# Kernel optimization log

Hardware: AMD Instinct MI355X
Metric: run time of the kernel (lower is better)

Reference implementation:

```python
import jax, jax.numpy as jnp
import numpy as np

NUM_EMBEDDINGS = 512
EMBEDDING_DIM = 64
COMMITMENT_COST = 0.25


def setup_inputs() -> dict:
    key = jax.random.key(0)
    k1, k2 = jax.random.split(key)
    inputs = jax.random.normal(k1, (16, EMBEDDING_DIM, 4096), dtype=jnp.float32)
    # torch init: uniform(-1/num_embeddings, 1/num_embeddings)
    codebook = jax.random.uniform(
        k2, (NUM_EMBEDDINGS, EMBEDDING_DIM), dtype=jnp.float32,
        minval=-1.0 / NUM_EMBEDDINGS, maxval=1.0 / NUM_EMBEDDINGS)
    return {"inputs": inputs, "codebook": codebook}


def reference(inputs, codebook):
    # inputs: [B, D, T] -> permute to [B, T, D]
    x = jnp.transpose(inputs, (0, 2, 1))
    B, T, D = x.shape
    K = codebook.shape[0]
    flat = x.reshape(-1, D)  # [N, D]

    distances = (jnp.sum(flat * flat, axis=1, keepdims=True)
                 + jnp.sum(codebook * codebook, axis=1)
                 - 2.0 * flat @ codebook.T)  # [N, K]
    idx = jnp.argmin(distances, axis=1)  # [N]
    encodings = jax.nn.one_hot(idx, K, dtype=jnp.float32)  # [N, K]

    # direct gather == encodings @ codebook
    quantized = codebook[idx].reshape(B, T, D)

    e_latent_loss = jnp.mean((jax.lax.stop_gradient(quantized) - x) ** 2)
    q_latent_loss = jnp.mean((quantized - jax.lax.stop_gradient(x)) ** 2)
    loss = q_latent_loss + COMMITMENT_COST * e_latent_loss

    # straight-through estimator
    quantized_st = x + jax.lax.stop_gradient(quantized - x)

    avg_probs = jnp.mean(encodings, axis=0)
    perplexity = jnp.exp(-jnp.sum(avg_probs * jnp.log(avg_probs + 1e-10)))

    return (loss, jnp.transpose(quantized_st, (0, 2, 1)), perplexity, encodings)
```

## Files before the change

kernel.cpp:

```cpp
#include <hip/hip_runtime.h>

#define B_ 16
#define D_ 64
#define T_ 4096
#define K_ 512
#define N_ (B_*T_)
#define Q_ (B_*D_*T_)
#define ENC_OFF ((size_t)(2 + Q_))

#define WS_LOSS    0
#define WS_HIST    16
#define WS_NE      2064
#define WS_CBH     4608
#define WS_CBL     70144

typedef __bf16 bf16x8 __attribute__((ext_vector_type(8)));
typedef float  f32x4  __attribute__((ext_vector_type(4)));

__global__ __launch_bounds__(256) void k0_init(const float* __restrict__ cb,
                                               float* __restrict__ ne,
                                               int* __restrict__ hist,
                                               double* __restrict__ loss,
                                               bf16x8* __restrict__ cbh,
                                               bf16x8* __restrict__ cbl) {
    int bidx = blockIdx.x, tid = threadIdx.x;

    if (tid < 64) {
        int code = bidx * 64 + tid;
        float s = 0.f;
#pragma unroll
        for (int d = 0; d < 64; ++d) { float c = cb[code*64 + d]; s = fmaf(c, c, s); }
        ne[code] = s;
    }
    if (bidx == 0) {
        hist[tid] = 0; hist[tid + 256] = 0;
        if (tid == 0) *loss = 0.0;
    }

#pragma unroll
    for (int p = 0; p < 2; ++p) {
        int e = p * 256 + tid;
        int ct = bidx * 4 + (e >> 7);
        int ks = (e >> 6) & 1;
        int lane = e & 63;
        int code  = ct * 16 + (lane & 15);
        int dbase = ks * 32 + ((lane >> 4) << 3);
        bf16x8 h, l;
#pragma unroll
        for (int j = 0; j < 8; ++j) {
            float v = cb[code * 64 + dbase + j];
            __bf16 hv = (__bf16)v;
            __bf16 lv = (__bf16)(v - (float)hv);
            h[j] = hv; l[j] = lv;
        }
        cbh[(ct * 2 + ks) * 64 + lane] = h;
        cbl[(ct * 2 + ks) * 64 + lane] = l;
    }
}

__global__ __launch_bounds__(256) void k_main(const float* __restrict__ in,
                                              const float* __restrict__ cb,
                                              const bf16x8* __restrict__ cbh,
                                              const bf16x8* __restrict__ cbl,
                                              const float* __restrict__ ne,
                                              float* __restrict__ out,
                                              float2* __restrict__ enc2,
                                              int* __restrict__ hist,
                                              double* __restrict__ loss) {
    __shared__ float X[64][65];
    __shared__ float ne_s[512];
    __shared__ int   sidx[64];
    int tid = threadIdx.x;
    int n0 = blockIdx.x * 64;
    int b  = n0 >> 12, t0 = n0 & (T_ - 1);

    {
        int tl = tid & 63, dg = tid >> 6;
#pragma unroll
        for (int i = 0; i < 16; ++i) {
            int d = dg * 16 + i;
            X[d][tl] = in[((size_t)b * 64 + d) * T_ + t0 + tl];
        }
    }
    ne_s[tid] = ne[tid];
    ne_s[tid + 256] = ne[tid + 256];
    __syncthreads();

    int w = tid >> 6, lane = tid & 63;
    int col = lane & 15, q = lane >> 4;

    bf16x8 Ah[2], Al[2];
#pragma unroll
    for (int ks = 0; ks < 2; ++ks) {
        bf16x8 h, l;
#pragma unroll
        for (int j = 0; j < 8; ++j) {
            float v = X[ks * 32 + q * 8 + j][w * 16 + col];
            __bf16 hv = (__bf16)v;
            __bf16 lv = (__bf16)(v - (float)hv);
            h[j] = hv; l[j] = lv;
        }
        Ah[ks] = h; Al[ks] = l;
    }

    float m1[4]; int i1[4];
#pragma unroll
    for (int e = 0; e < 4; ++e) { m1[e] = 3.4e38f; i1[e] = 0; }

    for (int ct = 0; ct < 32; ++ct) {
        bf16x8 Bh0 = cbh[(ct * 2 + 0) * 64 + lane];
        bf16x8 Bh1 = cbh[(ct * 2 + 1) * 64 + lane];
        bf16x8 Bl0 = cbl[(ct * 2 + 0) * 64 + lane];
        bf16x8 Bl1 = cbl[(ct * 2 + 1) * 64 + lane];
        float nev = ne_s[ct * 16 + col];
        int code = ct * 16 + col;
        f32x4 acc = {0.f, 0.f, 0.f, 0.f};
        acc = __builtin_amdgcn_mfma_f32_16x16x32_bf16(Ah[0], Bh0, acc, 0, 0, 0);
        acc = __builtin_amdgcn_mfma_f32_16x16x32_bf16(Ah[1], Bh1, acc, 0, 0, 0);
        acc = __builtin_amdgcn_mfma_f32_16x16x32_bf16(Ah[0], Bl0, acc, 0, 0, 0);
        acc = __builtin_amdgcn_mfma_f32_16x16x32_bf16(Al[0], Bh0, acc, 0, 0, 0);
        acc = __builtin_amdgcn_mfma_f32_16x16x32_bf16(Ah[1], Bl1, acc, 0, 0, 0);
        acc = __builtin_amdgcn_mfma_f32_16x16x32_bf16(Al[1], Bh1, acc, 0, 0, 0);
#pragma unroll
        for (int e = 0; e < 4; ++e) {
            float sc = fmaf(-2.f, acc[e], nev);
            bool lt = sc < m1[e];
            i1[e] = lt ? code : i1[e];
            m1[e] = lt ? sc : m1[e];
        }
    }

#pragma unroll
    for (int e = 0; e < 4; ++e) {
        float a1 = m1[e]; int ai = i1[e];
#pragma unroll
        for (int off = 1; off < 16; off <<= 1) {
            float o1 = __shfl_xor(a1, off);
            int   oi = __shfl_xor(ai, off);
            bool tk = (o1 < a1) || (o1 == a1 && oi < ai);
            a1 = tk ? o1 : a1; ai = tk ? oi : ai;
        }
        if (col == 0) sidx[w * 16 + q * 4 + e] = ai;
    }
    __syncthreads();

#pragma unroll 4
    for (int i = 0; i < 64; ++i) {
        int id = sidx[i];
        float2 v;
        v.x = ((id >> 1) == tid && (id & 1) == 0) ? 1.f : 0.f;
        v.y = ((id >> 1) == tid && (id & 1) == 1) ? 1.f : 0.f;
        enc2[(size_t)(n0 + i) * 256 + tid] = v;
    }

    int tl = tid & 63, dg = tid >> 6;
    int idq = sidx[tl];
    const float4* cq4 = (const float4*)(cb + (size_t)idq * 64 + dg * 16);
    float* qp = out + 1 + (size_t)b * D_ * T_ + (size_t)(dg * 16) * T_ + t0 + tl;

    float lsum = 0.f;
#pragma unroll
    for (int j4 = 0; j4 < 4; ++j4) {
        float4 qv = cq4[j4];
        float qe[4] = {qv.x, qv.y, qv.z, qv.w};
#pragma unroll
        for (int e = 0; e < 4; ++e) {
            int dl = j4 * 4 + e;
            float xv = X[dg * 16 + dl][tl];
            float diff = qe[e] - xv;
            lsum = fmaf(diff, diff, lsum);
            qp[(size_t)dl * T_] = xv + diff;
        }
    }
    if (tid < 64) atomicAdd(&hist[idq], 1);

#pragma unroll
    for (int off = 32; off > 0; off >>= 1) lsum += __shfl_down(lsum, off);
    __shared__ float wsum[4];
    if ((tid & 63) == 0) wsum[tid >> 6] = lsum;
    __syncthreads();
    if (tid == 0) {
        double s = (double)wsum[0] + (double)wsum[1] + (double)wsum[2] + (double)wsum[3];
        atomicAdd(loss, s);
    }
}

__global__ __launch_bounds__(512) void k6_final(const int* __restrict__ hist,
                                                const double* __restrict__ loss,
                                                float* __restrict__ out) {
    __shared__ double sh[512];
    int k = threadIdx.x;
    double p = (double)hist[k] / (double)N_;
    sh[k] = p * log(p + 1e-10);
    __syncthreads();
    for (int s = 256; s > 0; s >>= 1) {
        if (k < s) sh[k] += sh[k + s];
        __syncthreads();
    }
    if (k == 0) {
        out[1 + Q_] = (float)exp(-sh[0]);
        out[0] = (float)(1.25 * (*loss) / (double)Q_);
    }
}

extern "C" void kernel_launch(void* const* d_in, const int* in_sizes, int n_in,
                              void* d_out, int out_size, void* d_ws, size_t ws_size,
                              hipStream_t stream) {
    const float* in = (const float*)d_in[0];
    const float* cb = (const float*)d_in[1];
    float* out = (float*)d_out;
    char* ws = (char*)d_ws;

    double* loss  = (double*)(ws + WS_LOSS);
    int* hist     = (int*)(ws + WS_HIST);
    float* ne     = (float*)(ws + WS_NE);
    bf16x8* cbh   = (bf16x8*)(ws + WS_CBH);
    bf16x8* cbl   = (bf16x8*)(ws + WS_CBL);

    float2* enc2 = (float2*)(out + ENC_OFF);

    k0_init<<<8, 256, 0, stream>>>(cb, ne, hist, loss, cbh, cbl);
    k_main<<<N_ / 64, 256, 0, stream>>>(in, cb, cbh, cbl, ne, out, enc2, hist, loss);
    k6_final<<<1, 512, 0, stream>>>(hist, loss, out);
}
```

Baseline: 197.3 us.

## Replace global atomics with per-block partials and a final-kernel histogram

```diff
diff --git a/kernel.cpp b/kernel.cpp
--- a/kernel.cpp
+++ b/kernel.cpp
@@ -8,54 +8,44 @@
 #define Q_ (B_*D_*T_)
 #define ENC_OFF ((size_t)(2 + Q_))
 
-#define WS_LOSS    0
-#define WS_HIST    16
-#define WS_NE      2064
-#define WS_CBH     4608
-#define WS_CBL     70144
+#define WS_NE    0
+#define WS_LPART 2048
+#define WS_GIDX  6144
+#define WS_CBH   268288
+#define WS_CBL   333824
 
 typedef __bf16 bf16x8 __attribute__((ext_vector_type(8)));
 typedef float  f32x4  __attribute__((ext_vector_type(4)));
 
 __global__ __launch_bounds__(256) void k0_init(const float* __restrict__ cb,
                                                float* __restrict__ ne,
-                                               int* __restrict__ hist,
-                                               double* __restrict__ loss,
                                                bf16x8* __restrict__ cbh,
                                                bf16x8* __restrict__ cbl) {
     int bidx = blockIdx.x, tid = threadIdx.x;
 
-    if (tid < 64) {
-        int code = bidx * 64 + tid;
+    {
+        int code = bidx * 32 + (tid >> 3), sl = tid & 7;
         float s = 0.f;
 #pragma unroll
-        for (int d = 0; d < 64; ++d) { float c = cb[code*64 + d]; s = fmaf(c, c, s); }
-        ne[code] = s;
-    }
-    if (bidx == 0) {
-        hist[tid] = 0; hist[tid + 256] = 0;
-        if (tid == 0) *loss = 0.0;
-    }
-
-#pragma unroll
-    for (int p = 0; p < 2; ++p) {
-        int e = p * 256 + tid;
-        int ct = bidx * 4 + (e >> 7);
-        int ks = (e >> 6) & 1;
-        int lane = e & 63;
-        int code  = ct * 16 + (lane & 15);
-        int dbase = ks * 32 + ((lane >> 4) << 3);
-        bf16x8 h, l;
-#pragma unroll
-        for (int j = 0; j < 8; ++j) {
-            float v = cb[code * 64 + dbase + j];
-            __bf16 hv = (__bf16)v;
-            __bf16 lv = (__bf16)(v - (float)hv);
-            h[j] = hv; l[j] = lv;
-        }
-        cbh[(ct * 2 + ks) * 64 + lane] = h;
-        cbl[(ct * 2 + ks) * 64 + lane] = l;
-    }
+        for (int j = 0; j < 8; ++j) { float c = cb[code * 64 + sl * 8 + j]; s = fmaf(c, c, s); }
+        s += __shfl_xor(s, 1); s += __shfl_xor(s, 2); s += __shfl_xor(s, 4);
+        if (sl == 0) ne[code] = s;
+    }
+
+    int e = bidx * 256 + tid;
+    int ct = e >> 7, ks = (e >> 6) & 1, lane = e & 63;
+    int code  = ct * 16 + (lane & 15);
+    int dbase = ks * 32 + ((lane >> 4) << 3);
+    bf16x8 h, l;
+#pragma unroll
+    for (int j = 0; j < 8; ++j) {
+        float v = cb[code * 64 + dbase + j];
+        __bf16 hv = (__bf16)v;
+        __bf16 lv = (__bf16)(v - (float)hv);
+        h[j] = hv; l[j] = lv;
+    }
+    cbh[(ct * 2 + ks) * 64 + lane] = h;
+    cbl[(ct * 2 + ks) * 64 + lane] = l;
 }
 
 __global__ __launch_bounds__(256) void k_main(const float* __restrict__ in,
@@ -65,8 +55,8 @@
                                               const float* __restrict__ ne,
                                               float* __restrict__ out,
                                               float2* __restrict__ enc2,
-                                              int* __restrict__ hist,
-                                              double* __restrict__ loss) {
+                                              int* __restrict__ gidx,
+                                              float* __restrict__ lpart) {
     __shared__ float X[64][65];
     __shared__ float ne_s[512];
     __shared__ int   sidx[64];
@@ -172,34 +162,42 @@
             qp[(size_t)dl * T_] = xv + diff;
         }
     }
-    if (tid < 64) atomicAdd(&hist[idq], 1);
+    if (tid < 64) gidx[n0 + tid] = idq;
 
 #pragma unroll
     for (int off = 32; off > 0; off >>= 1) lsum += __shfl_down(lsum, off);
     __shared__ float wsum[4];
     if ((tid & 63) == 0) wsum[tid >> 6] = lsum;
     __syncthreads();
-    if (tid == 0) {
-        double s = (double)wsum[0] + (double)wsum[1] + (double)wsum[2] + (double)wsum[3];
-        atomicAdd(loss, s);
-    }
-}
-
-__global__ __launch_bounds__(512) void k6_final(const int* __restrict__ hist,
-                                                const double* __restrict__ loss,
+    if (tid == 0)
+        lpart[blockIdx.x] = wsum[0] + wsum[1] + wsum[2] + wsum[3];
+}
+
+__global__ __launch_bounds__(512) void k6_final(const int* __restrict__ gidx,
+                                                const float* __restrict__ lpart,
                                                 float* __restrict__ out) {
+    __shared__ int    h[512];
     __shared__ double sh[512];
+    __shared__ double sl2[512];
     int k = threadIdx.x;
-    double p = (double)hist[k] / (double)N_;
-    sh[k] = p * log(p + 1e-10);
+    h[k] = 0;
+    __syncthreads();
+#pragma unroll 4
+    for (int i = 0; i < 128; ++i)
+        atomicAdd(&h[gidx[(size_t)i * 512 + k]], 1);
+    double ls = (double)lpart[k] + (double)lpart[k + 512];
+    __syncthreads();
+    double p = (double)h[k] / (double)N_;
+    sh[k]  = p * log(p + 1e-10);
+    sl2[k] = ls;
     __syncthreads();
     for (int s = 256; s > 0; s >>= 1) {
-        if (k < s) sh[k] += sh[k + s];
+        if (k < s) { sh[k] += sh[k + s]; sl2[k] += sl2[k + s]; }
         __syncthreads();
     }
     if (k == 0) {
         out[1 + Q_] = (float)exp(-sh[0]);
-        out[0] = (float)(1.25 * (*loss) / (double)Q_);
+        out[0] = (float)(1.25 * sl2[0] / (double)Q_);
     }
 }
 
@@ -211,15 +209,15 @@
     float* out = (float*)d_out;
     char* ws = (char*)d_ws;
 
-    double* loss  = (double*)(ws + WS_LOSS);
-    int* hist     = (int*)(ws + WS_HIST);
     float* ne     = (float*)(ws + WS_NE);
+    float* lpart  = (float*)(ws + WS_LPART);
+    int*   gidx   = (int*)(ws + WS_GIDX);
     bf16x8* cbh   = (bf16x8*)(ws + WS_CBH);
     bf16x8* cbl   = (bf16x8*)(ws + WS_CBL);
 
     float2* enc2 = (float2*)(out + ENC_OFF);
 
-    k0_init<<<8, 256, 0, stream>>>(cb, ne, hist, loss, cbh, cbl);
-    k_main<<<N_ / 64, 256, 0, stream>>>(in, cb, cbh, cbl, ne, out, enc2, hist, loss);
-    k6_final<<<1, 512, 0, stream>>>(hist, loss, out);
-}
+    k0_init<<<16, 256, 0, stream>>>(cb, ne, cbh, cbl);
+    k_main<<<N_ / 64, 256, 0, stream>>>(in, cb, cbh, cbl, ne, out, enc2, gidx, lpart);
+    k6_final<<<1, 512, 0, stream>>>(gidx, lpart, out);
+}
```

Measured after the change: 216.3 us. 1.1x slower.

## Split codebook across waves and reuse B fragments over four row tiles

Applied to the files above, without the earlier changes.

```diff
diff --git a/kernel.cpp b/kernel.cpp
--- a/kernel.cpp
+++ b/kernel.cpp
@@ -25,37 +25,33 @@
                                                bf16x8* __restrict__ cbl) {
     int bidx = blockIdx.x, tid = threadIdx.x;
 
-    if (tid < 64) {
-        int code = bidx * 64 + tid;
+    {
+        int code = bidx * 32 + (tid >> 3), sl = tid & 7;
         float s = 0.f;
 #pragma unroll
-        for (int d = 0; d < 64; ++d) { float c = cb[code*64 + d]; s = fmaf(c, c, s); }
-        ne[code] = s;
+        for (int j = 0; j < 8; ++j) { float c = cb[code * 64 + sl * 8 + j]; s = fmaf(c, c, s); }
+        s += __shfl_xor(s, 1); s += __shfl_xor(s, 2); s += __shfl_xor(s, 4);
+        if (sl == 0) ne[code] = s;
     }
     if (bidx == 0) {
         hist[tid] = 0; hist[tid + 256] = 0;
         if (tid == 0) *loss = 0.0;
     }
 
-#pragma unroll
-    for (int p = 0; p < 2; ++p) {
-        int e = p * 256 + tid;
-        int ct = bidx * 4 + (e >> 7);
-        int ks = (e >> 6) & 1;
-        int lane = e & 63;
-        int code  = ct * 16 + (lane & 15);
-        int dbase = ks * 32 + ((lane >> 4) << 3);
-        bf16x8 h, l;
-#pragma unroll
-        for (int j = 0; j < 8; ++j) {
-            float v = cb[code * 64 + dbase + j];
-            __bf16 hv = (__bf16)v;
-            __bf16 lv = (__bf16)(v - (float)hv);
-            h[j] = hv; l[j] = lv;
-        }
-        cbh[(ct * 2 + ks) * 64 + lane] = h;
-        cbl[(ct * 2 + ks) * 64 + lane] = l;
-    }
+    int e = bidx * 256 + tid;
+    int ct = e >> 7, ks = (e >> 6) & 1, lane = e & 63;
+    int code  = ct * 16 + (lane & 15);
+    int dbase = ks * 32 + ((lane >> 4) << 3);
+    bf16x8 h, l;
+#pragma unroll
+    for (int j = 0; j < 8; ++j) {
+        float v = cb[code * 64 + dbase + j];
+        __bf16 hv = (__bf16)v;
+        __bf16 lv = (__bf16)(v - (float)hv);
+        h[j] = hv; l[j] = lv;
+    }
+    cbh[(ct * 2 + ks) * 64 + lane] = h;
+    cbl[(ct * 2 + ks) * 64 + lane] = l;
 }
 
 __global__ __launch_bounds__(256) void k_main(const float* __restrict__ in,
@@ -70,6 +66,8 @@
     __shared__ float X[64][65];
     __shared__ float ne_s[512];
     __shared__ int   sidx[64];
+    __shared__ float smin[4][64];
+    __shared__ int   smid[4][64];
     int tid = threadIdx.x;
     int n0 = blockIdx.x * 64;
     int b  = n0 >> 12, t0 = n0 & (T_ - 1);
@@ -89,58 +87,81 @@
     int w = tid >> 6, lane = tid & 63;
     int col = lane & 15, q = lane >> 4;
 
-    bf16x8 Ah[2], Al[2];
-#pragma unroll
-    for (int ks = 0; ks < 2; ++ks) {
-        bf16x8 h, l;
-#pragma unroll
-        for (int j = 0; j < 8; ++j) {
-            float v = X[ks * 32 + q * 8 + j][w * 16 + col];
-            __bf16 hv = (__bf16)v;
-            __bf16 lv = (__bf16)(v - (float)hv);
-            h[j] = hv; l[j] = lv;
-        }
-        Ah[ks] = h; Al[ks] = l;
-    }
-
-    float m1[4]; int i1[4];
-#pragma unroll
-    for (int e = 0; e < 4; ++e) { m1[e] = 3.4e38f; i1[e] = 0; }
-
-    for (int ct = 0; ct < 32; ++ct) {
+    bf16x8 Ah[4][2], Al[4][2];
+#pragma unroll
+    for (int mt = 0; mt < 4; ++mt)
+#pragma unroll
+        for (int ks = 0; ks < 2; ++ks) {
+            bf16x8 h, l;
+#pragma unroll
+            for (int j = 0; j < 8; ++j) {
+                float v = X[ks * 32 + q * 8 + j][mt * 16 + col];
+                __bf16 hv = (__bf16)v;
+                __bf16 lv = (__bf16)(v - (float)hv);
+                h[j] = hv; l[j] = lv;
+            }
+            Ah[mt][ks] = h; Al[mt][ks] = l;
+        }
+
+    float m1[4][4]; int i1[4][4];
+#pragma unroll
+    for (int mt = 0; mt < 4; ++mt)
+#pragma unroll
+        for (int e = 0; e < 4; ++e) { m1[mt][e] = 3.4e38f; i1[mt][e] = 0; }
+
+#pragma unroll 2
+    for (int c8 = 0; c8 < 8; ++c8) {
+        int ct = w * 8 + c8;
         bf16x8 Bh0 = cbh[(ct * 2 + 0) * 64 + lane];
         bf16x8 Bh1 = cbh[(ct * 2 + 1) * 64 + lane];
         bf16x8 Bl0 = cbl[(ct * 2 + 0) * 64 + lane];
         bf16x8 Bl1 = cbl[(ct * 2 + 1) * 64 + lane];
         float nev = ne_s[ct * 16 + col];
         int code = ct * 16 + col;
-        f32x4 acc = {0.f, 0.f, 0.f, 0.f};
-        acc = __builtin_amdgcn_mfma_f32_16x16x32_bf16(Ah[0], Bh0, acc, 0, 0, 0);
-        acc = __builtin_amdgcn_mfma_f32_16x16x32_bf16(Ah[1], Bh1, acc, 0, 0, 0);
-        acc = __builtin_amdgcn_mfma_f32_16x16x32_bf16(Ah[0], Bl0, acc, 0, 0, 0);
-        acc = __builtin_amdgcn_mfma_f32_16x16x32_bf16(Al[0], Bh0, acc, 0, 0, 0);
-        acc = __builtin_amdgcn_mfma_f32_16x16x32_bf16(Ah[1], Bl1, acc, 0, 0, 0);
-        acc = __builtin_amdgcn_mfma_f32_16x16x32_bf16(Al[1], Bh1, acc, 0, 0, 0);
+#pragma unroll
+        for (int mt = 0; mt < 4; ++mt) {
+            f32x4 acc = {0.f, 0.f, 0.f, 0.f};
+            acc = __builtin_amdgcn_mfma_f32_16x16x32_bf16(Ah[mt][0], Bh0, acc, 0, 0, 0);
+            acc = __builtin_amdgcn_mfma_f32_16x16x32_bf16(Ah[mt][1], Bh1, acc, 0, 0, 0);
+            acc = __builtin_amdgcn_mfma_f32_16x16x32_bf16(Ah[mt][0], Bl0, acc, 0, 0, 0);
+            acc = __builtin_amdgcn_mfma_f32_16x16x32_bf16(Al[mt][0], Bh0, acc, 0, 0, 0);
+            acc = __builtin_amdgcn_mfma_f32_16x16x32_bf16(Ah[mt][1], Bl1, acc, 0, 0, 0);
+            acc = __builtin_amdgcn_mfma_f32_16x16x32_bf16(Al[mt][1], Bh1, acc, 0, 0, 0);
+#pragma unroll
+            for (int e = 0; e < 4; ++e) {
+                float sc = fmaf(-2.f, acc[e], nev);
+                bool lt = sc < m1[mt][e];
+                i1[mt][e] = lt ? code : i1[mt][e];
+                m1[mt][e] = lt ? sc : m1[mt][e];
+            }
+        }
+    }
+
+#pragma unroll
+    for (int mt = 0; mt < 4; ++mt)
 #pragma unroll
         for (int e = 0; e < 4; ++e) {
-            float sc = fmaf(-2.f, acc[e], nev);
-            bool lt = sc < m1[e];
-            i1[e] = lt ? code : i1[e];
-            m1[e] = lt ? sc : m1[e];
-        }
-    }
-
-#pragma unroll
-    for (int e = 0; e < 4; ++e) {
-        float a1 = m1[e]; int ai = i1[e];
-#pragma unroll
-        for (int off = 1; off < 16; off <<= 1) {
-            float o1 = __shfl_xor(a1, off);
-            int   oi = __shfl_xor(ai, off);
+            float a1 = m1[mt][e]; int ai = i1[mt][e];
+#pragma unroll
+            for (int off = 1; off < 16; off <<= 1) {
+                float o1 = __shfl_xor(a1, off);
+                int   oi = __shfl_xor(ai, off);
+                bool tk = (o1 < a1) || (o1 == a1 && oi < ai);
+                a1 = tk ? o1 : a1; ai = tk ? oi : ai;
+            }
+            if (col == 0) { smin[w][mt * 16 + q * 4 + e] = a1; smid[w][mt * 16 + q * 4 + e] = ai; }
+        }
+    __syncthreads();
+
+    if (tid < 64) {
+        float a1 = smin[0][tid]; int ai = smid[0][tid];
+#pragma unroll
+        for (int w2 = 1; w2 < 4; ++w2) {
+            float o1 = smin[w2][tid]; int oi = smid[w2][tid];
             bool tk = (o1 < a1) || (o1 == a1 && oi < ai);
             a1 = tk ? o1 : a1; ai = tk ? oi : ai;
         }
-        if (col == 0) sidx[w * 16 + q * 4 + e] = ai;
+        sidx[tid] = ai;
     }
     __syncthreads();
 
@@ -219,7 +240,7 @@
 
     float2* enc2 = (float2*)(out + ENC_OFF);
 
-    k0_init<<<8, 256, 0, stream>>>(cb, ne, hist, loss, cbh, cbl);
+    k0_init<<<16, 256, 0, stream>>>(cb, ne, hist, loss, cbh, cbl);
     k_main<<<N_ / 64, 256, 0, stream>>>(in, cb, cbh, cbl, ne, out, enc2, hist, loss);
     k6_final<<<1, 512, 0, stream>>>(hist, loss, out);
 }
```

Measured after the change: 203.9 us. 1.03x slower.

## Split one-hot encoding write into bulk zero-fill kernel plus scattered ones

Applied to the files above, without the earlier changes.

```diff
diff --git a/kernel.cpp b/kernel.cpp
--- a/kernel.cpp
+++ b/kernel.cpp
@@ -7,6 +7,7 @@
 #define N_ (B_*T_)
 #define Q_ (B_*D_*T_)
 #define ENC_OFF ((size_t)(2 + Q_))
+#define NK_ ((size_t)N_ * K_)
 
 #define WS_LOSS    0
 #define WS_HIST    16
@@ -25,48 +26,56 @@
                                                bf16x8* __restrict__ cbl) {
     int bidx = blockIdx.x, tid = threadIdx.x;
 
-    if (tid < 64) {
-        int code = bidx * 64 + tid;
+    {
+        int code = bidx * 32 + (tid >> 3), sl = tid & 7;
         float s = 0.f;
 #pragma unroll
-        for (int d = 0; d < 64; ++d) { float c = cb[code*64 + d]; s = fmaf(c, c, s); }
-        ne[code] = s;
+        for (int j = 0; j < 8; ++j) { float c = cb[code * 64 + sl * 8 + j]; s = fmaf(c, c, s); }
+        s += __shfl_xor(s, 1); s += __shfl_xor(s, 2); s += __shfl_xor(s, 4);
+        if (sl == 0) ne[code] = s;
     }
     if (bidx == 0) {
         hist[tid] = 0; hist[tid + 256] = 0;
         if (tid == 0) *loss = 0.0;
     }
 
-#pragma unroll
-    for (int p = 0; p < 2; ++p) {
-        int e = p * 256 + tid;
-        int ct = bidx * 4 + (e >> 7);
-        int ks = (e >> 6) & 1;
-        int lane = e & 63;
-        int code  = ct * 16 + (lane & 15);
-        int dbase = ks * 32 + ((lane >> 4) << 3);
-        bf16x8 h, l;
-#pragma unroll
-        for (int j = 0; j < 8; ++j) {
-            float v = cb[code * 64 + dbase + j];
-            __bf16 hv = (__bf16)v;
-            __bf16 lv = (__bf16)(v - (float)hv);
-            h[j] = hv; l[j] = lv;
-        }
-        cbh[(ct * 2 + ks) * 64 + lane] = h;
-        cbl[(ct * 2 + ks) * 64 + lane] = l;
-    }
-}
-
-__global__ __launch_bounds__(256) void k_main(const float* __restrict__ in,
-                                              const float* __restrict__ cb,
-                                              const bf16x8* __restrict__ cbh,
-                                              const bf16x8* __restrict__ cbl,
-                                              const float* __restrict__ ne,
-                                              float* __restrict__ out,
-                                              float2* __restrict__ enc2,
-                                              int* __restrict__ hist,
-                                              double* __restrict__ loss) {
+    int e = bidx * 256 + tid;
+    int ct = e >> 7, ks = (e >> 6) & 1, lane = e & 63;
+    int code  = ct * 16 + (lane & 15);
+    int dbase = ks * 32 + ((lane >> 4) << 3);
+    bf16x8 h, l;
+#pragma unroll
+    for (int j = 0; j < 8; ++j) {
+        float v = cb[code * 64 + dbase + j];
+        __bf16 hv = (__bf16)v;
+        __bf16 lv = (__bf16)(v - (float)hv);
+        h[j] = hv; l[j] = lv;
+    }
+    cbh[(ct * 2 + ks) * 64 + lane] = h;
+    cbl[(ct * 2 + ks) * 64 + lane] = l;
+}
+
+__global__ __launch_bounds__(256) void k_zero(float* __restrict__ out) {
+    f32x4* p4 = (f32x4*)(out + ENC_OFF + 2);
+    const size_t n4 = (NK_ - 4) / 4;
+    f32x4 z = {0.f, 0.f, 0.f, 0.f};
+    size_t stride = (size_t)gridDim.x * 256;
+    for (size_t c = (size_t)blockIdx.x * 256 + threadIdx.x; c < n4; c += stride)
+        p4[c] = z;
+    if (blockIdx.x == 0 && threadIdx.x == 0) {
+        out[ENC_OFF] = 0.f;           out[ENC_OFF + 1] = 0.f;
+        out[ENC_OFF + NK_ - 2] = 0.f; out[ENC_OFF + NK_ - 1] = 0.f;
+    }
+}
+
+__global__ __launch_bounds__(256) void k_argmin(const float* __restrict__ in,
+                                                const float* __restrict__ cb,
+                                                const bf16x8* __restrict__ cbh,
+                                                const bf16x8* __restrict__ cbl,
+                                                const float* __restrict__ ne,
+                                                float* __restrict__ out,
+                                                int* __restrict__ hist,
+                                                double* __restrict__ loss) {
     __shared__ float X[64][65];
     __shared__ float ne_s[512];
     __shared__ int   sidx[64];
@@ -144,15 +153,6 @@
     }
     __syncthreads();
 
-#pragma unroll 4
-    for (int i = 0; i < 64; ++i) {
-        int id = sidx[i];
-        float2 v;
-        v.x = ((id >> 1) == tid && (id & 1) == 0) ? 1.f : 0.f;
-        v.y = ((id >> 1) == tid && (id & 1) == 1) ? 1.f : 0.f;
-        enc2[(size_t)(n0 + i) * 256 + tid] = v;
-    }
-
     int tl = tid & 63, dg = tid >> 6;
     int idq = sidx[tl];
     const float4* cq4 = (const float4*)(cb + (size_t)idq * 64 + dg * 16);
@@ -172,7 +172,11 @@
             qp[(size_t)dl * T_] = xv + diff;
         }
     }
-    if (tid < 64) atomicAdd(&hist[idq], 1);
+    if (tid < 64) {
+        int id = sidx[tid];
+        out[ENC_OFF + (size_t)(n0 + tid) * K_ + id] = 1.0f;
+        atomicAdd(&hist[id], 1);
+    }
 
 #pragma unroll
     for (int off = 32; off > 0; off >>= 1) lsum += __shfl_down(lsum, off);
@@ -217,9 +221,8 @@
     bf16x8* cbh   = (bf16x8*)(ws + WS_CBH);
     bf16x8* cbl   = (bf16x8*)(ws + WS_CBL);
 
-    float2* enc2 = (float2*)(out + ENC_OFF);
-
-    k0_init<<<8, 256, 0, stream>>>(cb, ne, hist, loss, cbh, cbl);
-    k_main<<<N_ / 64, 256, 0, stream>>>(in, cb, cbh, cbl, ne, out, enc2, hist, loss);
+    k0_init<<<16, 256, 0, stream>>>(cb, ne, hist, loss, cbh, cbl);
+    k_zero<<<2048, 256, 0, stream>>>(out);
+    k_argmin<<<N_ / 64, 256, 0, stream>>>(in, cb, cbh, cbl, ne, out, hist, loss);
     k6_final<<<1, 512, 0, stream>>>(hist, loss, out);
 }
```

Measured after the change: 218.5 us. 1.11x slower.
